# Kernel optimization log

Hardware: AMD Instinct MI355X
Metric: run time of the kernel (lower is better)

## Reference

```python
import jax, jax.numpy as jnp
import numpy as np


def _grid_sample_3d(inp, grid):
    # Trilinear grid_sample, padding_mode='zeros', align_corners=True.
    # inp:  (B, C, D0, D1, D2)  (torch layout: grid[...,0] -> last dim D2,
    #                            grid[...,1] -> D1, grid[...,2] -> D0)
    # grid: (B, G0, G1, G2, 3), normalized coords in [-1, 1]
    B, C, D0, D1, D2 = inp.shape
    G0, G1, G2 = grid.shape[1:4]
    K = G0 * G1 * G2
    gx = (grid[..., 0] + 1.0) * 0.5 * (D2 - 1)
    gy = (grid[..., 1] + 1.0) * 0.5 * (D1 - 1)
    gz = (grid[..., 2] + 1.0) * 0.5 * (D0 - 1)
    x0 = jnp.floor(gx); y0 = jnp.floor(gy); z0 = jnp.floor(gz)
    tx = gx - x0; ty = gy - y0; tz = gz - z0
    x0i = x0.astype(jnp.int32); y0i = y0.astype(jnp.int32); z0i = z0.astype(jnp.int32)
    flat = inp.reshape(B, C, D0 * D1 * D2)
    out = jnp.zeros((B, C, K), inp.dtype)
    for dz in (0, 1):
        for dy in (0, 1):
            for dx in (0, 1):
                ix = x0i + dx; iy = y0i + dy; iz = z0i + dz
                w = ((tx if dx else 1.0 - tx)
                     * (ty if dy else 1.0 - ty)
                     * (tz if dz else 1.0 - tz))
                valid = ((ix >= 0) & (ix < D2) & (iy >= 0) & (iy < D1)
                         & (iz >= 0) & (iz < D0))
                ixc = jnp.clip(ix, 0, D2 - 1)
                iyc = jnp.clip(iy, 0, D1 - 1)
                izc = jnp.clip(iz, 0, D0 - 1)
                lin = ((izc * D1 + iyc) * D2 + ixc).reshape(B, 1, K)
                v = jnp.take_along_axis(flat, lin, axis=2)  # (B, C, K)
                out = out + v * (w * valid).reshape(B, 1, K).astype(inp.dtype)
    return out.reshape(B, C, G0, G1, G2)


def setup_inputs() -> dict:
    key = jax.random.key(0)
    k1, k2, k3 = jax.random.split(key, 3)
    B, N, C, W, H, D = 1, 6, 64, 48, 32, 88
    Z, Y, X = 16, 160, 160
    frustum_features = jax.random.normal(k1, (B, N, C, W, H, D), jnp.float32)
    # slightly outside [-1,1] to exercise zero padding, like real projections
    grid = jax.random.uniform(k2, (B * N, Z, Y, X, 3), jnp.float32,
                              minval=-1.1, maxval=1.1)
    mask = jax.random.bernoulli(k3, 0.3, (B * N, Z, Y, X))
    return {"frustum_features": frustum_features, "grid": grid, "mask": mask}


def reference(frustum_features, grid, mask):
    B, N, C, W, H, D = frustum_features.shape
    vox = _grid_sample_3d(frustum_features.reshape(B * N, C, W, H, D), grid)
    # voxel_features[mask] = 0  (mask broadcast over channel dim)
    vox = jnp.where(mask[:, None, :, :, :], jnp.zeros((), vox.dtype), vox)
    vox = vox.reshape(B, N, C, *vox.shape[2:]).sum(axis=1)  # sum over views
    # permute (B, C, Z, Y, X) -> (B, C, X, Y, Z)
    return jnp.transpose(vox, (0, 1, 4, 3, 2))
```

## Files before the change

kernel.cpp:

```cpp
#include <hip/hip_runtime.h>
#include <hip/hip_fp16.h>

constexpr int N_ = 6;
constexpr int C_ = 64;
constexpr int D0 = 48;
constexpr int D1 = 32;
constexpr int D2 = 88;
constexpr int P_ = D0 * D1 * D2;
constexpr int Z_ = 16, Y_ = 160, X_ = 160;
constexpr int NP_ = N_ * Z_ * Y_ * X_;

__device__ inline unsigned pkh(float a, float b) {
    __half2 h = __floats2half2_rn(a, b);
    return *reinterpret_cast<unsigned*>(&h);
}
__device__ inline float2 uph(unsigned u) {
    __half2 h = *reinterpret_cast<__half2*>(&u);
    return __half22float2(h);
}

__global__ __launch_bounds__(256) void k_transpose_h(const float* __restrict__ in,
                                                     __half* __restrict__ out) {
    __shared__ float lds[64][65];
    const int n  = blockIdx.y;
    const int p0 = blockIdx.x * 64;
    const int t  = threadIdx.x;
    const float* ip = in + (size_t)n * C_ * P_;
    __half*      op = out + (size_t)n * P_ * C_;

    const int pq = t & 15;
    const int cb = t >> 4;
#pragma unroll
    for (int i = 0; i < 4; ++i) {
        const int c = i * 16 + cb;
        const float4 v = *reinterpret_cast<const float4*>(ip + (size_t)c * P_ + p0 + pq * 4);
        lds[pq * 4 + 0][c] = v.x;
        lds[pq * 4 + 1][c] = v.y;
        lds[pq * 4 + 2][c] = v.z;
        lds[pq * 4 + 3][c] = v.w;
    }
    __syncthreads();
    const int c0 = (t & 7) * 8;
    const int pr = t >> 3;
#pragma unroll
    for (int i = 0; i < 2; ++i) {
        const int p = i * 32 + pr;
        uint4 u;
        u.x = pkh(lds[p][c0 + 0], lds[p][c0 + 1]);
        u.y = pkh(lds[p][c0 + 2], lds[p][c0 + 3]);
        u.z = pkh(lds[p][c0 + 4], lds[p][c0 + 5]);
        u.w = pkh(lds[p][c0 + 6], lds[p][c0 + 7]);
        *reinterpret_cast<uint4*>(op + (size_t)(p0 + p) * C_ + c0) = u;
    }
}

__global__ __launch_bounds__(256) void k_pre(const float* __restrict__ grid,
                                             const int* __restrict__ mask,
                                             uint4* __restrict__ S) {
    const int pidx = blockIdx.x * 256 + threadIdx.x;
    const float* g = grid + (size_t)pidx * 3;
    const float gx = (g[0] + 1.f) * (0.5f * (D2 - 1));
    const float gy = (g[1] + 1.f) * (0.5f * (D1 - 1));
    const float gz = (g[2] + 1.f) * (0.5f * (D0 - 1));
    const float fx = floorf(gx), fy = floorf(gy), fz = floorf(gz);
    const float tx = gx - fx, ty = gy - fy, tz = gz - fz;
    const int x0 = (int)fx, y0 = (int)fy, z0 = (int)fz;
    const int x1 = x0 + 1, y1 = y0 + 1, z1 = z0 + 1;
    const bool skip = (mask[pidx] != 0)
                   || x1 < 0 || x0 > D2 - 1 || y1 < 0 || y0 > D1 - 1
                   || z1 < 0 || z0 > D0 - 1;
    const float vx0 = (x0 >= 0)      ? (1.f - tx) : 0.f;
    const float vx1 = (x1 <= D2 - 1) ? tx         : 0.f;
    const float vy0 = (y0 >= 0)      ? (1.f - ty) : 0.f;
    const float vy1 = (y1 <= D1 - 1) ? ty         : 0.f;
    const float vz0 = (z0 >= 0)      ? (1.f - tz) : 0.f;
    const float vz1 = (z1 <= D0 - 1) ? tz         : 0.f;
    const int xc0 = max(x0, 0),  xc1 = min(x1, D2 - 1);
    const int yc0 = max(y0, 0),  yc1 = min(y1, D1 - 1);
    const int zc0 = max(z0, 0),  zc1 = min(z1, D0 - 1);
    const int n = pidx / (Z_ * Y_ * X_);
    const unsigned base = (unsigned)(n * P_);
    const unsigned q00 = base + (zc0 * D1 + yc0) * D2 + xc0;
    const unsigned q01 = base + (zc0 * D1 + yc1) * D2 + xc0;
    const unsigned q10 = base + (zc1 * D1 + yc0) * D2 + xc0;
    const unsigned q11 = base + (zc1 * D1 + yc1) * D2 + xc0;
    const unsigned dx = (unsigned)(xc1 - xc0);
    const float w00 = vz0 * vy0, w01 = vz0 * vy1;
    const float w10 = vz1 * vy0, w11 = vz1 * vy1;
    uint4 A = make_uint4(q00 | (dx << 30) | (skip ? 0x80000000u : 0u), q01, q10, q11);
    uint4 B = make_uint4(pkh(vx0 * w00, vx1 * w00), pkh(vx0 * w01, vx1 * w01),
                         pkh(vx0 * w10, vx1 * w10), pkh(vx0 * w11, vx1 * w11));
    S[(size_t)pidx * 2 + 0] = A;
    S[(size_t)pidx * 2 + 1] = B;
}

__global__ __launch_bounds__(256) void k_sample3(const __half* __restrict__ feat,
                                                 const uint4* __restrict__ S,
                                                 float* __restrict__ outp) {
    const int x    = blockIdx.x;
    const int y0   = blockIdx.y * 4;
    const int lane = threadIdx.x;
    const int wv   = threadIdx.y;
    const int y    = __builtin_amdgcn_readfirstlane(y0 + wv);

    float acc[16];
#pragma unroll
    for (int i = 0; i < 16; ++i) acc[i] = 0.f;

    const char* fc = reinterpret_cast<const char*>(feat);

#pragma unroll
    for (int z = 0; z < Z_; ++z) {
        for (int n = 0; n < N_; ++n) {
            const int pidx = ((n * Z_ + z) * Y_ + y) * X_ + x;
            const uint4 A = S[(size_t)pidx * 2 + 0];
            if (A.x & 0x80000000u) continue;
            const uint4 B = S[(size_t)pidx * 2 + 1];
            const unsigned dxb = ((A.x >> 30) & 1u) << 7;
            const unsigned o00 = (A.x & 0x000FFFFFu) << 7;
            const unsigned o01 = A.y << 7;
            const unsigned o10 = A.z << 7;
            const unsigned o11 = A.w << 7;
            const float2 w0 = uph(B.x), w1 = uph(B.y), w2 = uph(B.z), w3 = uph(B.w);
            float s;
            s  = __half2float(reinterpret_cast<const __half*>(fc + o00)[lane])       * w0.x;
            s += __half2float(reinterpret_cast<const __half*>(fc + o00 + dxb)[lane]) * w0.y;
            s += __half2float(reinterpret_cast<const __half*>(fc + o01)[lane])       * w1.x;
            s += __half2float(reinterpret_cast<const __half*>(fc + o01 + dxb)[lane]) * w1.y;
            s += __half2float(reinterpret_cast<const __half*>(fc + o10)[lane])       * w2.x;
            s += __half2float(reinterpret_cast<const __half*>(fc + o10 + dxb)[lane]) * w2.y;
            s += __half2float(reinterpret_cast<const __half*>(fc + o11)[lane])       * w3.x;
            s += __half2float(reinterpret_cast<const __half*>(fc + o11 + dxb)[lane]) * w3.y;
            acc[z] += s;
        }
    }

    __shared__ float lds[64][65];
#pragma unroll
    for (int z = 0; z < 16; ++z)
        lds[wv * 16 + z][lane] = acc[z];
    __syncthreads();
    const size_t obase = (size_t)y0 * Z_ + (size_t)x * (Y_ * Z_);
#pragma unroll
    for (int i = 0; i < 16; ++i) {
        const int c = i * 4 + wv;
        outp[(size_t)c * (X_ * Y_ * Z_) + obase + lane] = lds[lane][c];
    }
}

__global__ __launch_bounds__(256) void k_sample_raw(const float* __restrict__ feat,
                                                    const float* __restrict__ grid,
                                                    const int* __restrict__ mask,
                                                    float* __restrict__ outp) {
    const int x    = blockIdx.x;
    const int y0   = blockIdx.y * 4;
    const int lane = threadIdx.x;
    const int wv   = threadIdx.y;
    const int y    = y0 + wv;
    float acc[16];
#pragma unroll
    for (int i = 0; i < 16; ++i) acc[i] = 0.f;
    for (int n = 0; n < N_; ++n) {
        const float* fb = feat + ((size_t)n * C_ + lane) * P_;
        for (int z = 0; z < Z_; ++z) {
            const int pidx = ((n * Z_ + z) * Y_ + y) * X_ + x;
            if (mask[pidx]) continue;
            const float* g = grid + (size_t)pidx * 3;
            const float gx = (g[0] + 1.f) * (0.5f * (D2 - 1));
            const float gy = (g[1] + 1.f) * (0.5f * (D1 - 1));
            const float gz = (g[2] + 1.f) * (0.5f * (D0 - 1));
            const float fx = floorf(gx), fy = floorf(gy), fz = floorf(gz);
            const float tx = gx - fx, ty = gy - fy, tz = gz - fz;
            const int x0 = (int)fx, y0i = (int)fy, z0i = (int)fz;
            const int x1 = x0 + 1, y1 = y0i + 1, z1 = z0i + 1;
            if (x1 < 0 || x0 > D2 - 1 || y1 < 0 || y0i > D1 - 1 ||
                z1 < 0 || z0i > D0 - 1) continue;
            const float vx0 = (x0 >= 0)      ? (1.f - tx) : 0.f;
            const float vx1 = (x1 <= D2 - 1) ? tx         : 0.f;
            const float vy0 = (y0i >= 0)     ? (1.f - ty) : 0.f;
            const float vy1 = (y1 <= D1 - 1) ? ty         : 0.f;
            const float vz0 = (z0i >= 0)     ? (1.f - tz) : 0.f;
            const float vz1 = (z1 <= D0 - 1) ? tz         : 0.f;
            const int xc0 = max(x0, 0),  xc1 = min(x1, D2 - 1);
            const int yc0 = max(y0i, 0), yc1 = min(y1, D1 - 1);
            const int zc0 = max(z0i, 0), zc1 = min(z1, D0 - 1);
            const int r00 = (zc0 * D1 + yc0) * D2;
            const int r01 = (zc0 * D1 + yc1) * D2;
            const int r10 = (zc1 * D1 + yc0) * D2;
            const int r11 = (zc1 * D1 + yc1) * D2;
            const float w00 = vz0 * vy0, w01 = vz0 * vy1;
            const float w10 = vz1 * vy0, w11 = vz1 * vy1;
            acc[z] += (fb[r00 + xc0] * vx0 + fb[r00 + xc1] * vx1) * w00
                    + (fb[r01 + xc0] * vx0 + fb[r01 + xc1] * vx1) * w01
                    + (fb[r10 + xc0] * vx0 + fb[r10 + xc1] * vx1) * w10
                    + (fb[r11 + xc0] * vx0 + fb[r11 + xc1] * vx1) * w11;
        }
    }
    __shared__ float lds[64][65];
#pragma unroll
    for (int z = 0; z < 16; ++z)
        lds[wv * 16 + z][lane] = acc[z];
    __syncthreads();
    const size_t obase = (size_t)y0 * Z_ + (size_t)x * (Y_ * Z_);
#pragma unroll
    for (int i = 0; i < 16; ++i) {
        const int c = i * 4 + wv;
        outp[(size_t)c * (X_ * Y_ * Z_) + obase + lane] = lds[lane][c];
    }
}

extern "C" void kernel_launch(void* const* d_in, const int* in_sizes, int n_in,
                              void* d_out, int out_size, void* d_ws, size_t ws_size,
                              hipStream_t stream) {
    const float* feat = (const float*)d_in[0];
    const float* grid = (const float*)d_in[1];
    const int*   mask = (const int*)d_in[2];
    float*       outp = (float*)d_out;

    const size_t featT_bytes = (size_t)N_ * P_ * C_ * sizeof(__half);
    const size_t S_bytes     = (size_t)NP_ * 32;
    if (ws_size >= featT_bytes + S_bytes) {
        __half* featT = (__half*)d_ws;
        uint4*  S     = (uint4*)((char*)d_ws + featT_bytes);
        k_transpose_h<<<dim3(P_ / 64, N_), 256, 0, stream>>>(feat, featT);
        k_pre<<<NP_ / 256, 256, 0, stream>>>(grid, mask, S);
        k_sample3<<<dim3(X_, Y_ / 4), dim3(64, 4), 0, stream>>>(featT, S, outp);
    } else {
        k_sample_raw<<<dim3(X_, Y_ / 4), dim3(64, 4), 0, stream>>>(feat, grid, mask, outp);
    }
}
```

Before: 633.3 us.

## Compress sample descriptors to 16 bytes and merge preprocessing kernels

Fuses the feature transpose and grid preprocessing into one launch, with the block index choosing the role. Each sample's descriptor shrinks from 32 to 16 bytes: it now holds a single base offset with dx/dy/dz step bits and three factored half2 weights, and the sampler recomputes the eight corner addresses and weight products. The sampler loop order changes to n-outer, z-inner. This halves descriptor write and read traffic and removes one launch, at the cost of a few extra multiplies per sample and a different fp16 rounding of the separable weights.

After: 594.2 us. 1.07x faster.

```diff
diff --git a/kernel.cpp b/kernel.cpp
--- a/kernel.cpp
+++ b/kernel.cpp
@@ -10,6 +10,10 @@
 constexpr int Z_ = 16, Y_ = 160, X_ = 160;
 constexpr int NP_ = N_ * Z_ * Y_ * X_;
 
+constexpr int TP_BLOCKS_PER_N = P_ / 64;
+constexpr int TP_BLOCKS = TP_BLOCKS_PER_N * N_;
+constexpr int PRE_BLOCKS = NP_ / 256;
+
 __device__ inline unsigned pkh(float a, float b) {
     __half2 h = __floats2half2_rn(a, b);
     return *reinterpret_cast<unsigned*>(&h);
@@ -19,82 +23,79 @@
     return __half22float2(h);
 }
 
-__global__ __launch_bounds__(256) void k_transpose_h(const float* __restrict__ in,
-                                                     __half* __restrict__ out) {
-    __shared__ float lds[64][65];
-    const int n  = blockIdx.y;
-    const int p0 = blockIdx.x * 64;
-    const int t  = threadIdx.x;
-    const float* ip = in + (size_t)n * C_ * P_;
-    __half*      op = out + (size_t)n * P_ * C_;
-
-    const int pq = t & 15;
-    const int cb = t >> 4;
-#pragma unroll
-    for (int i = 0; i < 4; ++i) {
-        const int c = i * 16 + cb;
-        const float4 v = *reinterpret_cast<const float4*>(ip + (size_t)c * P_ + p0 + pq * 4);
-        lds[pq * 4 + 0][c] = v.x;
-        lds[pq * 4 + 1][c] = v.y;
-        lds[pq * 4 + 2][c] = v.z;
-        lds[pq * 4 + 3][c] = v.w;
-    }
-    __syncthreads();
-    const int c0 = (t & 7) * 8;
-    const int pr = t >> 3;
-#pragma unroll
-    for (int i = 0; i < 2; ++i) {
-        const int p = i * 32 + pr;
-        uint4 u;
-        u.x = pkh(lds[p][c0 + 0], lds[p][c0 + 1]);
-        u.y = pkh(lds[p][c0 + 2], lds[p][c0 + 3]);
-        u.z = pkh(lds[p][c0 + 4], lds[p][c0 + 5]);
-        u.w = pkh(lds[p][c0 + 6], lds[p][c0 + 7]);
-        *reinterpret_cast<uint4*>(op + (size_t)(p0 + p) * C_ + c0) = u;
-    }
-}
-
-__global__ __launch_bounds__(256) void k_pre(const float* __restrict__ grid,
+__global__ __launch_bounds__(256) void k_aux(const float* __restrict__ in,
+                                             __half* __restrict__ out,
+                                             const float* __restrict__ grid,
                                              const int* __restrict__ mask,
                                              uint4* __restrict__ S) {
-    const int pidx = blockIdx.x * 256 + threadIdx.x;
-    const float* g = grid + (size_t)pidx * 3;
-    const float gx = (g[0] + 1.f) * (0.5f * (D2 - 1));
-    const float gy = (g[1] + 1.f) * (0.5f * (D1 - 1));
-    const float gz = (g[2] + 1.f) * (0.5f * (D0 - 1));
-    const float fx = floorf(gx), fy = floorf(gy), fz = floorf(gz);
-    const float tx = gx - fx, ty = gy - fy, tz = gz - fz;
-    const int x0 = (int)fx, y0 = (int)fy, z0 = (int)fz;
-    const int x1 = x0 + 1, y1 = y0 + 1, z1 = z0 + 1;
-    const bool skip = (mask[pidx] != 0)
-                   || x1 < 0 || x0 > D2 - 1 || y1 < 0 || y0 > D1 - 1
-                   || z1 < 0 || z0 > D0 - 1;
-    const float vx0 = (x0 >= 0)      ? (1.f - tx) : 0.f;
-    const float vx1 = (x1 <= D2 - 1) ? tx         : 0.f;
-    const float vy0 = (y0 >= 0)      ? (1.f - ty) : 0.f;
-    const float vy1 = (y1 <= D1 - 1) ? ty         : 0.f;
-    const float vz0 = (z0 >= 0)      ? (1.f - tz) : 0.f;
-    const float vz1 = (z1 <= D0 - 1) ? tz         : 0.f;
-    const int xc0 = max(x0, 0),  xc1 = min(x1, D2 - 1);
-    const int yc0 = max(y0, 0),  yc1 = min(y1, D1 - 1);
-    const int zc0 = max(z0, 0),  zc1 = min(z1, D0 - 1);
-    const int n = pidx / (Z_ * Y_ * X_);
-    const unsigned base = (unsigned)(n * P_);
-    const unsigned q00 = base + (zc0 * D1 + yc0) * D2 + xc0;
-    const unsigned q01 = base + (zc0 * D1 + yc1) * D2 + xc0;
-    const unsigned q10 = base + (zc1 * D1 + yc0) * D2 + xc0;
-    const unsigned q11 = base + (zc1 * D1 + yc1) * D2 + xc0;
-    const unsigned dx = (unsigned)(xc1 - xc0);
-    const float w00 = vz0 * vy0, w01 = vz0 * vy1;
-    const float w10 = vz1 * vy0, w11 = vz1 * vy1;
-    uint4 A = make_uint4(q00 | (dx << 30) | (skip ? 0x80000000u : 0u), q01, q10, q11);
-    uint4 B = make_uint4(pkh(vx0 * w00, vx1 * w00), pkh(vx0 * w01, vx1 * w01),
-                         pkh(vx0 * w10, vx1 * w10), pkh(vx0 * w11, vx1 * w11));
-    S[(size_t)pidx * 2 + 0] = A;
-    S[(size_t)pidx * 2 + 1] = B;
-}
-
-__global__ __launch_bounds__(256) void k_sample3(const __half* __restrict__ feat,
+    const int t = threadIdx.x;
+    if (blockIdx.x < TP_BLOCKS) {
+        __shared__ float lds[64][65];
+        const int n  = blockIdx.x / TP_BLOCKS_PER_N;
+        const int p0 = (blockIdx.x % TP_BLOCKS_PER_N) * 64;
+        const float* ip = in + (size_t)n * C_ * P_;
+        __half*      op = out + (size_t)n * P_ * C_;
+        const int pq = t & 15;
+        const int cb = t >> 4;
+#pragma unroll
+        for (int i = 0; i < 4; ++i) {
+            const int c = i * 16 + cb;
+            const float4 v = *reinterpret_cast<const float4*>(ip + (size_t)c * P_ + p0 + pq * 4);
+            lds[pq * 4 + 0][c] = v.x;
+            lds[pq * 4 + 1][c] = v.y;
+            lds[pq * 4 + 2][c] = v.z;
+            lds[pq * 4 + 3][c] = v.w;
+        }
+        __syncthreads();
+        const int c0 = (t & 7) * 8;
+        const int pr = t >> 3;
+#pragma unroll
+        for (int i = 0; i < 2; ++i) {
+            const int p = i * 32 + pr;
+            uint4 u;
+            u.x = pkh(lds[p][c0 + 0], lds[p][c0 + 1]);
+            u.y = pkh(lds[p][c0 + 2], lds[p][c0 + 3]);
+            u.z = pkh(lds[p][c0 + 4], lds[p][c0 + 5]);
+            u.w = pkh(lds[p][c0 + 6], lds[p][c0 + 7]);
+            *reinterpret_cast<uint4*>(op + (size_t)(p0 + p) * C_ + c0) = u;
+        }
+    } else {
+        const int pidx = (blockIdx.x - TP_BLOCKS) * 256 + t;
+        const float* g = grid + (size_t)pidx * 3;
+        const float gx = (g[0] + 1.f) * (0.5f * (D2 - 1));
+        const float gy = (g[1] + 1.f) * (0.5f * (D1 - 1));
+        const float gz = (g[2] + 1.f) * (0.5f * (D0 - 1));
+        const float fx = floorf(gx), fy = floorf(gy), fz = floorf(gz);
+        const float tx = gx - fx, ty = gy - fy, tz = gz - fz;
+        const int x0 = (int)fx, y0 = (int)fy, z0 = (int)fz;
+        const int x1 = x0 + 1, y1 = y0 + 1, z1 = z0 + 1;
+        const bool skip = (mask[pidx] != 0)
+                       || x1 < 0 || x0 > D2 - 1 || y1 < 0 || y0 > D1 - 1
+                       || z1 < 0 || z0 > D0 - 1;
+        const float vx0 = (x0 >= 0)      ? (1.f - tx) : 0.f;
+        const float vx1 = (x1 <= D2 - 1) ? tx         : 0.f;
+        const float vy0 = (y0 >= 0)      ? (1.f - ty) : 0.f;
+        const float vy1 = (y1 <= D1 - 1) ? ty         : 0.f;
+        const float vz0 = (z0 >= 0)      ? (1.f - tz) : 0.f;
+        const float vz1 = (z1 <= D0 - 1) ? tz         : 0.f;
+        const int xc0 = max(x0, 0),  xc1 = min(x1, D2 - 1);
+        const int yc0 = max(y0, 0),  yc1 = min(y1, D1 - 1);
+        const int zc0 = max(z0, 0),  zc1 = min(z1, D0 - 1);
+        const int n = pidx / (Z_ * Y_ * X_);
+        const unsigned q00 = (unsigned)(n * P_) + (zc0 * D1 + yc0) * D2 + xc0;
+        const unsigned dx = (unsigned)(xc1 - xc0);
+        const unsigned dy = (unsigned)(yc1 - yc0);
+        const unsigned dz = (unsigned)(zc1 - zc0);
+        uint4 Dsc;
+        Dsc.x = q00 | (dx << 20) | (dy << 21) | (dz << 22) | (skip ? 0x80000000u : 0u);
+        Dsc.y = pkh(vx0, vx1);
+        Dsc.z = pkh(vz0 * vy0, vz0 * vy1);
+        Dsc.w = pkh(vz1 * vy0, vz1 * vy1);
+        S[pidx] = Dsc;
+    }
+}
+
+__global__ __launch_bounds__(256) void k_sample4(const __half* __restrict__ feat,
                                                  const uint4* __restrict__ S,
                                                  float* __restrict__ outp) {
     const int x    = blockIdx.x;
@@ -109,28 +110,32 @@
 
     const char* fc = reinterpret_cast<const char*>(feat);
 
-#pragma unroll
-    for (int z = 0; z < Z_; ++z) {
-        for (int n = 0; n < N_; ++n) {
+    for (int n = 0; n < N_; ++n) {
+#pragma unroll
+        for (int z = 0; z < Z_; ++z) {
             const int pidx = ((n * Z_ + z) * Y_ + y) * X_ + x;
-            const uint4 A = S[(size_t)pidx * 2 + 0];
+            const uint4 A = S[pidx];
             if (A.x & 0x80000000u) continue;
-            const uint4 B = S[(size_t)pidx * 2 + 1];
-            const unsigned dxb = ((A.x >> 30) & 1u) << 7;
             const unsigned o00 = (A.x & 0x000FFFFFu) << 7;
-            const unsigned o01 = A.y << 7;
-            const unsigned o10 = A.z << 7;
-            const unsigned o11 = A.w << 7;
-            const float2 w0 = uph(B.x), w1 = uph(B.y), w2 = uph(B.z), w3 = uph(B.w);
+            const unsigned dxb = ((A.x >> 20) & 1u) << 7;
+            const unsigned dyb = ((A.x >> 21) & 1u) ? (unsigned)(D2 * 128) : 0u;
+            const unsigned dzb = ((A.x >> 22) & 1u) ? (unsigned)(D1 * D2 * 128) : 0u;
+            const float2 wx = uph(A.y);
+            const float2 wa = uph(A.z);
+            const float2 wb = uph(A.w);
+            const char* p00 = fc + o00;
+            const char* p01 = p00 + dyb;
+            const char* p10 = p00 + dzb;
+            const char* p11 = p10 + dyb;
             float s;
-            s  = __half2float(reinterpret_cast<const __half*>(fc + o00)[lane])       * w0.x;
-            s += __half2float(reinterpret_cast<const __half*>(fc + o00 + dxb)[lane]) * w0.y;
-            s += __half2float(reinterpret_cast<const __half*>(fc + o01)[lane])       * w1.x;
-            s += __half2float(reinterpret_cast<const __half*>(fc + o01 + dxb)[lane]) * w1.y;
-            s += __half2float(reinterpret_cast<const __half*>(fc + o10)[lane])       * w2.x;
-            s += __half2float(reinterpret_cast<const __half*>(fc + o10 + dxb)[lane]) * w2.y;
-            s += __half2float(reinterpret_cast<const __half*>(fc + o11)[lane])       * w3.x;
-            s += __half2float(reinterpret_cast<const __half*>(fc + o11 + dxb)[lane]) * w3.y;
+            s  = __half2float(reinterpret_cast<const __half*>(p00)[lane])               * (wx.x * wa.x);
+            s += __half2float(reinterpret_cast<const __half*>(p00 + dxb)[lane])         * (wx.y * wa.x);
+            s += __half2float(reinterpret_cast<const __half*>(p01)[lane])               * (wx.x * wa.y);
+            s += __half2float(reinterpret_cast<const __half*>(p01 + dxb)[lane])         * (wx.y * wa.y);
+            s += __half2float(reinterpret_cast<const __half*>(p10)[lane])               * (wx.x * wb.x);
+            s += __half2float(reinterpret_cast<const __half*>(p10 + dxb)[lane])         * (wx.y * wb.x);
+            s += __half2float(reinterpret_cast<const __half*>(p11)[lane])               * (wx.x * wb.y);
+            s += __half2float(reinterpret_cast<const __half*>(p11 + dxb)[lane])         * (wx.y * wb.y);
             acc[z] += s;
         }
     }
@@ -218,13 +223,12 @@
     float*       outp = (float*)d_out;
 
     const size_t featT_bytes = (size_t)N_ * P_ * C_ * sizeof(__half);
-    const size_t S_bytes     = (size_t)NP_ * 32;
+    const size_t S_bytes     = (size_t)NP_ * 16;
     if (ws_size >= featT_bytes + S_bytes) {
         __half* featT = (__half*)d_ws;
         uint4*  S     = (uint4*)((char*)d_ws + featT_bytes);
-        k_transpose_h<<<dim3(P_ / 64, N_), 256, 0, stream>>>(feat, featT);
-        k_pre<<<NP_ / 256, 256, 0, stream>>>(grid, mask, S);
-        k_sample3<<<dim3(X_, Y_ / 4), dim3(64, 4), 0, stream>>>(featT, S, outp);
+        k_aux<<<TP_BLOCKS + PRE_BLOCKS, 256, 0, stream>>>(feat, featT, grid, mask, S);
+        k_sample4<<<dim3(X_, Y_ / 4), dim3(64, 4), 0, stream>>>(featT, S, outp);
     } else {
         k_sample_raw<<<dim3(X_, Y_ / 4), dim3(64, 4), 0, stream>>>(feat, grid, mask, outp);
     }
```
